# Optimization experiments

Measured on AMD Instinct MI355X. Metric: run time of the kernel, lower is better.

Reference implementation:

```python
import jax, jax.numpy as jnp
import numpy as np

B, S, HID = 8, 1024, 1024
NH, HD = 16, 64  # num heads, head dim; NH*HD == HID


def setup_inputs() -> dict:
    key = jax.random.key(0)
    ks = jax.random.split(key, 8)
    sc = 0.02
    return {
        "hidden_states": jax.random.normal(ks[0], (B, S, HID), jnp.float32),
        "attention_mask": jnp.zeros((B, 1, 1, S), jnp.float32),
        "Wq": jax.random.normal(ks[1], (HID, HID), jnp.float32) * sc,
        "bq": jnp.zeros((HID,), jnp.float32),
        "Wk": jax.random.normal(ks[2], (HID, HID), jnp.float32) * sc,
        "bk": jnp.zeros((HID,), jnp.float32),
        "Wv": jax.random.normal(ks[3], (HID, HID), jnp.float32) * sc,
        "bv": jnp.zeros((HID,), jnp.float32),
    }


def reference(hidden_states, attention_mask, Wq, bq, Wk, bk, Wv, bv):
    def split_heads(x):  # [B,S,HID] -> [B,NH,S,HD]
        return x.reshape(B, S, NH, HD).transpose(0, 2, 1, 3)

    q = split_heads(hidden_states @ Wq + bq)
    k = split_heads(hidden_states @ Wk + bk)
    v = split_heads(hidden_states @ Wv + bv)

    # [B,NH,S,S] score matrix, scale, additive mask, softmax
    scores = jnp.einsum("bhqd,bhkd->bhqk", q, k) / jnp.sqrt(jnp.float32(HD))
    scores = scores + attention_mask
    probs = jax.nn.softmax(scores, axis=-1)  # dropout prob = 0.0 -> identity

    ctx = jnp.einsum("bhqk,bhkd->bhqd", probs, v)
    return ctx.transpose(0, 2, 1, 3).reshape(B, S, HID)
```

## Files before the change

### kernel.cpp

```cpp
#include <hip/hip_runtime.h>


typedef __bf16 bf16x8 __attribute__((ext_vector_type(8)));
typedef float f32x4 __attribute__((ext_vector_type(4)));
typedef float f32x16 __attribute__((ext_vector_type(16)));

__device__ __forceinline__ unsigned rne16(float x) {
  unsigned u = __builtin_bit_cast(unsigned, x);
  return (u + 0x7fffu + ((u >> 16) & 1u)) >> 16;
}
__device__ __forceinline__ unsigned packbf(float lo, float hi) {
  return rne16(lo) | (rne16(hi) << 16);
}
__device__ __forceinline__ unsigned packbf_fast(float lo, float hi) {
  unsigned ul = __builtin_bit_cast(unsigned, lo) + 0x8000u;
  unsigned uh = __builtin_bit_cast(unsigned, hi) + 0x8000u;
  return __builtin_amdgcn_perm(uh, ul, 0x07060302u);
}
__device__ __forceinline__ void async16(void* l, const void* g) {
  __builtin_amdgcn_global_load_lds((const __attribute__((address_space(1))) void*)g,
                                   (__attribute__((address_space(3))) void*)l, 16, 0, 0);
}

__global__ __launch_bounds__(256) void k_prep(const float* __restrict__ h,
                                              unsigned short* __restrict__ hbf,
                                              const float* __restrict__ Wq,
                                              const float* __restrict__ Wk,
                                              const float* __restrict__ Wv,
                                              unsigned short* __restrict__ wt) {
  __shared__ float t[32][33];
  int bid = blockIdx.x, tid = threadIdx.x;
  if (bid < 8192) {
    size_t i = (size_t)bid * 256 + tid;
    float4 v = ((const float4*)h)[i];
    uint2 r;
    r.x = packbf(v.x, v.y);
    r.y = packbf(v.z, v.w);
    ((uint2*)hbf)[i] = r;
  } else {
    int id = bid - 8192;
    int which = id >> 10;
    int sub = id & 1023;
    int c0 = (sub & 31) * 32, k0 = (sub >> 5) * 32;
    const float* W = which == 0 ? Wq : (which == 1 ? Wk : Wv);
    int tx = tid & 31, ty = tid >> 5;
#pragma unroll
    for (int i = 0; i < 4; ++i) {
      int r = ty + i * 8;
      t[r][tx] = W[(size_t)(k0 + r) * 1024 + c0 + tx];
    }
    __syncthreads();
#pragma unroll
    for (int i = 0; i < 4; ++i) {
      int r = ty + i * 8;
      wt[((size_t)which * 1024 + c0 + r) * 1024 + k0 + tx] = (unsigned short)rne16(t[tx][r]);
    }
  }
}

__global__ __launch_bounds__(256, 2) void k_gemm(const unsigned short* __restrict__ A,
                                                 const unsigned short* __restrict__ Bm,
                                                 const float* __restrict__ bq,
                                                 const float* __restrict__ bk,
                                                 const float* __restrict__ bv,
                                                 unsigned short* __restrict__ qkv,
                                                 unsigned short* __restrict__ vt) {
  __shared__ __align__(16) char lds[65536];
  const int tid = threadIdx.x;
  const int w = tid >> 6, lane = tid & 63;
  const int wm = w >> 1, wn = w & 1;

  int orig = blockIdx.x;
  int wgid = (orig & 7) * 64 + (orig >> 3);
  int tm = wgid >> 3, tn = wgid & 7;
  int m0 = tm * 128, n0 = tn * 384;

  int ro[6], ke[6];
#pragma unroll
  for (int j = 0; j < 6; ++j) {
    int o = j * 4096 + tid * 16;
    int s = o >> 10, w10 = o & 1023;
    int lg = w10 ^ (((w10 >> 9) & 1) << 5);
    ro[j] = s * 16 + (lg >> 6);
    ke[j] = (lg & 63) >> 1;
  }
  auto stage = [&](int kt, char* buf) {
    const unsigned short* As = A + (size_t)m0 * 1024 + kt * 32;
    const unsigned short* Bs = Bm + (size_t)n0 * 1024 + kt * 32;
#pragma unroll
    for (int j = 0; j < 2; ++j)
      async16(buf + j * 4096 + tid * 16, As + (size_t)ro[j] * 1024 + ke[j]);
#pragma unroll
    for (int j = 0; j < 6; ++j)
      async16(buf + 8192 + j * 4096 + tid * 16, Bs + (size_t)ro[j] * 1024 + ke[j]);
  };

  const int lswz = (((lane & 15) << 6) | ((lane >> 4) << 4)) ^ ((lane & 8) << 2);

  f32x4 acc[4][12];
#pragma unroll
  for (int i = 0; i < 4; ++i)
#pragma unroll
    for (int j = 0; j < 12; ++j)
#pragma unroll
      for (int e = 0; e < 4; ++e) acc[i][j][e] = 0.f;

  auto compute = [&](const char* buf) {
    const char* abase = buf + lswz;
    const char* bbase = buf + 8192 + lswz;
    bf16x8 aF[4];
#pragma unroll
    for (int mt = 0; mt < 4; ++mt)
      aF[mt] = *(const bf16x8*)(abase + ((size_t)(wm * 4 + mt) << 10));
#pragma unroll
    for (int n = 0; n < 12; ++n) {
      bf16x8 bF = *(const bf16x8*)(bbase + ((size_t)(wn * 12 + n) << 10));
#pragma unroll
      for (int mt = 0; mt < 4; ++mt)
        acc[mt][n] =
            __builtin_amdgcn_mfma_f32_16x16x32_bf16(aF[mt], bF, acc[mt][n], 0, 0, 0);
    }
  };

  char* buf0 = lds;
  char* buf1 = lds + 32768;
  stage(0, buf0);
#pragma unroll 1
  for (int kt = 0; kt < 32; kt += 2) {
    __syncthreads();
    stage(kt + 1, buf1);
    compute(buf0);
    __syncthreads();
    if (kt + 2 < 32) stage(kt + 2, buf0);
    compute(buf1);
  }

  const int b = m0 >> 10;
  const int r = lane & 15, qq = lane >> 4;
  const int sb = (m0 & 1023) + wm * 64 + qq * 4;
#pragma unroll
  for (int n = 0; n < 12; ++n) {
    int n_gf = n0 + wn * 192 + n * 16;
    int which = n_gf >> 10;
    int n_in = (n_gf & 1023) + r;
    if (which != 2) {
      const float* bp = which == 0 ? bq : bk;
      float bias = bp[n_in];
      unsigned short* dp = qkv + ((size_t)which << 23) + ((size_t)b << 20) +
                           ((size_t)(n_in >> 6) << 16) + (n_in & 63);
#pragma unroll
      for (int m = 0; m < 4; ++m)
#pragma unroll
        for (int e = 0; e < 4; ++e)
          dp[(size_t)(sb + m * 16 + e) << 6] = (unsigned short)rne16(acc[m][n][e] + bias);
    } else {
      float bias = bv[n_in];
      unsigned short* dp = vt + ((size_t)b << 20) + ((size_t)n_in << 10) + sb;
#pragma unroll
      for (int m = 0; m < 4; ++m) {
        uint2 pk;
        pk.x = packbf(acc[m][n][0] + bias, acc[m][n][1] + bias);
        pk.y = packbf(acc[m][n][2] + bias, acc[m][n][3] + bias);
        *(uint2*)(dp + m * 16) = pk;
      }
    }
  }
}

__global__ __launch_bounds__(256, 2) void k_attn(const unsigned short* __restrict__ qg,
                                                 const unsigned short* __restrict__ kg,
                                                 const unsigned short* __restrict__ vtg,
                                                 const float* __restrict__ maskg,
                                                 float* __restrict__ out) {
  __shared__ __align__(16) char lds[36864];
  float* MK = (float*)(lds + 32768);
  int tid = threadIdx.x, w = tid >> 6, lane = tid & 63, l5 = lane & 31, q5 = lane >> 5;
  int idx = blockIdx.x;
  int bi = idx & 7;
  int j = idx >> 3;
  int h = j >> 2, qc = j & 3;
  int bh = bi * 16 + h, s0 = qc * 256;
  const unsigned short* qb = qg + ((size_t)bh << 16);
  const unsigned short* kb = kg + ((size_t)bh << 16);
  const unsigned short* vb = vtg + ((size_t)bh << 16);
  const float LG = 1.4426950408889634f;
  const float C1 = 0.125f * LG;

  {
    float4 mv = *(const float4*)(maskg + (size_t)bi * 1024 + tid * 4);
    mv.x *= LG; mv.y *= LG; mv.z *= LG; mv.w *= LG;
    *(float4*)(MK + tid * 4) = mv;
  }

  auto stageKV = [&](int kt, char* buf) {
    int k0 = kt * 64;
#pragma unroll
    for (int t = 0; t < 2; ++t) {
      int f = w * 2 + t;
      int mt = f >> 2, ds = f & 3;
      async16(buf + f * 1024, kb + (size_t)(k0 + mt * 32 + l5) * 64 + ds * 16 + q5 * 8);
      int dt = f >> 2, ks = f & 3;
      async16(buf + 8192 + f * 1024,
              vb + (size_t)(dt * 32 + l5) * 1024 + k0 + ks * 16 + q5 * 8);
    }
  };

  bf16x8 qfr[2][4];
#pragma unroll
  for (int qh = 0; qh < 2; ++qh)
#pragma unroll
    for (int ds = 0; ds < 4; ++ds)
      qfr[qh][ds] = *(const bf16x8*)(qb + (size_t)(s0 + w * 64 + qh * 32 + l5) * 64 +
                                     ds * 16 + q5 * 8);

  f32x16 O[2][2];
#pragma unroll
  for (int qh = 0; qh < 2; ++qh)
#pragma unroll
    for (int i = 0; i < 2; ++i)
#pragma unroll
      for (int e = 0; e < 16; ++e) O[qh][i][e] = 0.f;
  float lsum0 = 0.f, lsum1 = 0.f;

  stageKV(0, lds);
  __syncthreads();

#pragma unroll 1
  for (int kt = 0; kt < 16; ++kt) {
    char* buf = lds + (kt & 1) * 16384;
    if (kt < 15) stageKV(kt + 1, lds + ((kt + 1) & 1) * 16384);
    int k0 = kt * 64;
    const char* KF = buf;
    const char* VF = buf + 8192;
#pragma unroll
    for (int mt = 0; mt < 2; ++mt) {
      f32x16 S0, S1;
#pragma unroll
      for (int e = 0; e < 16; ++e) { S0[e] = 0.f; S1[e] = 0.f; }
#pragma unroll
      for (int ds = 0; ds < 4; ++ds) {
        bf16x8 a = *(const bf16x8*)(KF + (mt * 4 + ds) * 1024 + lane * 16);
        S0 = __builtin_amdgcn_mfma_f32_32x32x16_bf16(a, qfr[0][ds], S0, 0, 0, 0);
        S1 = __builtin_amdgcn_mfma_f32_32x32x16_bf16(a, qfr[1][ds], S1, 0, 0, 0);
      }
      unsigned p2a[8], p2b[8];
      {
        float p[16];
#pragma unroll
        for (int g4 = 0; g4 < 4; ++g4) {
          float4 mv = *(const float4*)(MK + k0 + mt * 32 + g4 * 8 + q5 * 4);
          p[g4 * 4 + 0] = __builtin_amdgcn_exp2f(S0[g4 * 4 + 0] * C1 + mv.x);
          p[g4 * 4 + 1] = __builtin_amdgcn_exp2f(S0[g4 * 4 + 1] * C1 + mv.y);
          p[g4 * 4 + 2] = __builtin_amdgcn_exp2f(S0[g4 * 4 + 2] * C1 + mv.z);
          p[g4 * 4 + 3] = __builtin_amdgcn_exp2f(S0[g4 * 4 + 3] * C1 + mv.w);
        }
#pragma unroll
        for (int e = 0; e < 16; ++e) lsum0 += p[e];
#pragma unroll
        for (int jj = 0; jj < 8; ++jj) p2a[jj] = packbf_fast(p[2 * jj], p[2 * jj + 1]);
      }
      {
        float p[16];
#pragma unroll
        for (int g4 = 0; g4 < 4; ++g4) {
          float4 mv = *(const float4*)(MK + k0 + mt * 32 + g4 * 8 + q5 * 4);
          p[g4 * 4 + 0] = __builtin_amdgcn_exp2f(S1[g4 * 4 + 0] * C1 + mv.x);
          p[g4 * 4 + 1] = __builtin_amdgcn_exp2f(S1[g4 * 4 + 1] * C1 + mv.y);
          p[g4 * 4 + 2] = __builtin_amdgcn_exp2f(S1[g4 * 4 + 2] * C1 + mv.z);
          p[g4 * 4 + 3] = __builtin_amdgcn_exp2f(S1[g4 * 4 + 3] * C1 + mv.w);
        }
#pragma unroll
        for (int e = 0; e < 16; ++e) lsum1 += p[e];
#pragma unroll
        for (int jj = 0; jj < 8; ++jj) p2b[jj] = packbf_fast(p[2 * jj], p[2 * jj + 1]);
      }
#pragma unroll
      for (int kh = 0; kh < 2; ++kh) {
        int ks = mt * 2 + kh, gp = kh * 4;
        bf16x8 av0 = *(const bf16x8*)(VF + (0 * 4 + ks) * 1024 + lane * 16);
        bf16x8 av1 = *(const bf16x8*)(VF + (1 * 4 + ks) * 1024 + lane * 16);
        {
          unsigned o0 = p2a[gp + 0], o1 = p2a[gp + 1];
          unsigned o2 = p2a[gp + 2], o3 = p2a[gp + 3];
          unsigned t0 = __shfl_xor((int)o0, 32);
          unsigned t1 = __shfl_xor((int)o1, 32);
          unsigned t2 = __shfl_xor((int)o2, 32);
          unsigned t3 = __shfl_xor((int)o3, 32);
          uint4 fu;
          fu.x = q5 ? t2 : o0;
          fu.y = q5 ? t3 : o1;
          fu.z = q5 ? o2 : t0;
          fu.w = q5 ? o3 : t1;
          bf16x8 bfrag = __builtin_bit_cast(bf16x8, fu);
          O[0][0] = __builtin_amdgcn_mfma_f32_32x32x16_bf16(av0, bfrag, O[0][0], 0, 0, 0);
          O[0][1] = __builtin_amdgcn_mfma_f32_32x32x16_bf16(av1, bfrag, O[0][1], 0, 0, 0);
        }
        {
          unsigned o0 = p2b[gp + 0], o1 = p2b[gp + 1];
          unsigned o2 = p2b[gp + 2], o3 = p2b[gp + 3];
          unsigned t0 = __shfl_xor((int)o0, 32);
          unsigned t1 = __shfl_xor((int)o1, 32);
          unsigned t2 = __shfl_xor((int)o2, 32);
          unsigned t3 = __shfl_xor((int)o3, 32);
          uint4 fu;
          fu.x = q5 ? t2 : o0;
          fu.y = q5 ? t3 : o1;
          fu.z = q5 ? o2 : t0;
          fu.w = q5 ? o3 : t1;
          bf16x8 bfrag = __builtin_bit_cast(bf16x8, fu);
          O[1][0] = __builtin_amdgcn_mfma_f32_32x32x16_bf16(av0, bfrag, O[1][0], 0, 0, 0);
          O[1][1] = __builtin_amdgcn_mfma_f32_32x32x16_bf16(av1, bfrag, O[1][1], 0, 0, 0);
        }
      }
    }
    __syncthreads();
  }

  float* Ob = (float*)(lds + w * 8192);
  float lt0 = lsum0 + __shfl_xor(lsum0, 32);
  float lt1 = lsum1 + __shfl_xor(lsum1, 32);
  float rinv0 = 1.0f / lt0;
  float rinv1 = 1.0f / lt1;
#pragma unroll
  for (int qh = 0; qh < 2; ++qh) {
    float rinv = qh ? rinv1 : rinv0;
#pragma unroll
    for (int dt = 0; dt < 2; ++dt)
#pragma unroll
      for (int g4 = 0; g4 < 4; ++g4) {
        float4 val;
        val.x = O[qh][dt][g4 * 4 + 0] * rinv;
        val.y = O[qh][dt][g4 * 4 + 1] * rinv;
        val.z = O[qh][dt][g4 * 4 + 2] * rinv;
        val.w = O[qh][dt][g4 * 4 + 3] * rinv;
        int c = dt * 8 + g4 * 2 + q5;
        *(float4*)(Ob + l5 * 64 + (c ^ (l5 & 15)) * 4) = val;
      }
#pragma unroll
    for (int t = 0; t < 8; ++t) {
      int qr = t * 4 + (lane >> 4), cr = lane & 15;
      float4 vv = *(const float4*)(Ob + qr * 64 + (cr ^ (qr & 15)) * 4);
      int s = s0 + w * 64 + qh * 32 + qr;
      *(float4*)(out + (((size_t)(bi * 1024 + s)) << 10) + (h << 6) + (cr << 2)) = vv;
    }
  }
}

extern "C" void kernel_launch(void* const* d_in, const int* in_sizes, int n_in,
                              void* d_out, int out_size, void* d_ws, size_t ws_size,
                              hipStream_t stream) {
  (void)in_sizes; (void)n_in; (void)out_size; (void)ws_size;
  const float* hidden = (const float*)d_in[0];
  const float* mask = (const float*)d_in[1];
  const float* Wq = (const float*)d_in[2];
  const float* bq = (const float*)d_in[3];
  const float* Wk = (const float*)d_in[4];
  const float* bk = (const float*)d_in[5];
  const float* Wv = (const float*)d_in[6];
  const float* bv = (const float*)d_in[7];
  float* out = (float*)d_out;
  char* ws = (char*)d_ws;
  unsigned short* hbf = (unsigned short*)ws;
  unsigned short* wt  = (unsigned short*)(ws + 16777216);
  unsigned short* qkv = (unsigned short*)(ws + 23068672);
  unsigned short* vt  = (unsigned short*)(ws + 56623104);

  k_prep<<<11264, 256, 0, stream>>>(hidden, hbf, Wq, Wk, Wv, wt);
  k_gemm<<<512, 256, 0, stream>>>(hbf, wt, bq, bk, bv, qkv, vt);
  k_attn<<<512, 256, 0, stream>>>(qkv, qkv + 8388608, vt, mask, out);
}
```

Baseline: 210.3 us.

## Fuse hidden-state bf16 conversion into QKV GEMM A-tile loading

Drops the separate pass that converts hidden states to bf16 in the prep kernel. The GEMM now loads fp32 A tiles straight into registers, packs them to bf16 and writes them to LDS, overlapped with compute on the other buffer. This removes one write and one read of a 16MB intermediate and shrinks the prep grid. The cost is that A traffic inside the GEMM doubles (fp32 instead of bf16), each tile is re-read by the 8 N-tile blocks, and the A path uses synchronous register loads instead of async LDS loads, which adds register pressure.

```diff
diff --git a/kernel.cpp b/kernel.cpp
--- a/kernel.cpp
+++ b/kernel.cpp
@@ -22,43 +22,31 @@
                                    (__attribute__((address_space(3))) void*)l, 16, 0, 0);
 }
 
-__global__ __launch_bounds__(256) void k_prep(const float* __restrict__ h,
-                                              unsigned short* __restrict__ hbf,
-                                              const float* __restrict__ Wq,
+__global__ __launch_bounds__(256) void k_prep(const float* __restrict__ Wq,
                                               const float* __restrict__ Wk,
                                               const float* __restrict__ Wv,
                                               unsigned short* __restrict__ wt) {
   __shared__ float t[32][33];
-  int bid = blockIdx.x, tid = threadIdx.x;
-  if (bid < 8192) {
-    size_t i = (size_t)bid * 256 + tid;
-    float4 v = ((const float4*)h)[i];
-    uint2 r;
-    r.x = packbf(v.x, v.y);
-    r.y = packbf(v.z, v.w);
-    ((uint2*)hbf)[i] = r;
-  } else {
-    int id = bid - 8192;
-    int which = id >> 10;
-    int sub = id & 1023;
-    int c0 = (sub & 31) * 32, k0 = (sub >> 5) * 32;
-    const float* W = which == 0 ? Wq : (which == 1 ? Wk : Wv);
-    int tx = tid & 31, ty = tid >> 5;
-#pragma unroll
-    for (int i = 0; i < 4; ++i) {
-      int r = ty + i * 8;
-      t[r][tx] = W[(size_t)(k0 + r) * 1024 + c0 + tx];
-    }
-    __syncthreads();
-#pragma unroll
-    for (int i = 0; i < 4; ++i) {
-      int r = ty + i * 8;
-      wt[((size_t)which * 1024 + c0 + r) * 1024 + k0 + tx] = (unsigned short)rne16(t[tx][r]);
-    }
-  }
-}
-
-__global__ __launch_bounds__(256, 2) void k_gemm(const unsigned short* __restrict__ A,
+  int id = blockIdx.x, tid = threadIdx.x;
+  int which = id >> 10;
+  int sub = id & 1023;
+  int c0 = (sub & 31) * 32, k0 = (sub >> 5) * 32;
+  const float* W = which == 0 ? Wq : (which == 1 ? Wk : Wv);
+  int tx = tid & 31, ty = tid >> 5;
+#pragma unroll
+  for (int i = 0; i < 4; ++i) {
+    int r = ty + i * 8;
+    t[r][tx] = W[(size_t)(k0 + r) * 1024 + c0 + tx];
+  }
+  __syncthreads();
+#pragma unroll
+  for (int i = 0; i < 4; ++i) {
+    int r = ty + i * 8;
+    wt[((size_t)which * 1024 + c0 + r) * 1024 + k0 + tx] = (unsigned short)rne16(t[tx][r]);
+  }
+}
+
+__global__ __launch_bounds__(256, 2) void k_gemm(const float* __restrict__ h,
                                                  const unsigned short* __restrict__ Bm,
                                                  const float* __restrict__ bq,
                                                  const float* __restrict__ bk,
@@ -84,15 +72,32 @@
     ro[j] = s * 16 + (lg >> 6);
     ke[j] = (lg & 63) >> 1;
   }
-  auto stage = [&](int kt, char* buf) {
-    const unsigned short* As = A + (size_t)m0 * 1024 + kt * 32;
+  auto stageB = [&](int kt, char* buf) {
     const unsigned short* Bs = Bm + (size_t)n0 * 1024 + kt * 32;
-#pragma unroll
-    for (int j = 0; j < 2; ++j)
-      async16(buf + j * 4096 + tid * 16, As + (size_t)ro[j] * 1024 + ke[j]);
 #pragma unroll
     for (int j = 0; j < 6; ++j)
       async16(buf + 8192 + j * 4096 + tid * 16, Bs + (size_t)ro[j] * 1024 + ke[j]);
+  };
+  float4 aU[2], aV[2];
+  auto loadA = [&](int kt) {
+    const float* As = h + (size_t)m0 * 1024 + kt * 32;
+#pragma unroll
+    for (int j = 0; j < 2; ++j) {
+      const float* p = As + (size_t)ro[j] * 1024 + ke[j];
+      aU[j] = *(const float4*)(p);
+      aV[j] = *(const float4*)(p + 4);
+    }
+  };
+  auto writeA = [&](char* buf) {
+#pragma unroll
+    for (int j = 0; j < 2; ++j) {
+      uint4 pk;
+      pk.x = packbf(aU[j].x, aU[j].y);
+      pk.y = packbf(aU[j].z, aU[j].w);
+      pk.z = packbf(aV[j].x, aV[j].y);
+      pk.w = packbf(aV[j].z, aV[j].w);
+      *(uint4*)(buf + j * 4096 + tid * 16) = pk;
+    }
   };
 
   const int lswz = (((lane & 15) << 6) | ((lane >> 4) << 4)) ^ ((lane & 8) << 2);
@@ -124,15 +129,23 @@
 
   char* buf0 = lds;
   char* buf1 = lds + 32768;
-  stage(0, buf0);
+  loadA(0);
+  stageB(0, buf0);
+  writeA(buf0);
 #pragma unroll 1
   for (int kt = 0; kt < 32; kt += 2) {
     __syncthreads();
-    stage(kt + 1, buf1);
+    loadA(kt + 1);
+    stageB(kt + 1, buf1);
     compute(buf0);
+    writeA(buf1);
     __syncthreads();
-    if (kt + 2 < 32) stage(kt + 2, buf0);
+    if (kt + 2 < 32) {
+      loadA(kt + 2);
+      stageB(kt + 2, buf0);
+    }
     compute(buf1);
+    if (kt + 2 < 32) writeA(buf0);
   }
 
   const int b = m0 >> 10;
@@ -360,12 +373,11 @@
   const float* bv = (const float*)d_in[7];
   float* out = (float*)d_out;
   char* ws = (char*)d_ws;
-  unsigned short* hbf = (unsigned short*)ws;
   unsigned short* wt  = (unsigned short*)(ws + 16777216);
   unsigned short* qkv = (unsigned short*)(ws + 23068672);
   unsigned short* vt  = (unsigned short*)(ws + 56623104);
 
-  k_prep<<<11264, 256, 0, stream>>>(hidden, hbf, Wq, Wk, Wv, wt);
-  k_gemm<<<512, 256, 0, stream>>>(hbf, wt, bq, bk, bv, qkv, vt);
+  k_prep<<<3072, 256, 0, stream>>>(Wq, Wk, Wv, wt);
+  k_gemm<<<512, 256, 0, stream>>>(hidden, wt, bq, bk, bv, qkv, vt);
   k_attn<<<512, 256, 0, stream>>>(qkv, qkv + 8388608, vt, mask, out);
 }
```

Result: slower. 239.0 us (+13.7%).
